# Kernel tuning notes

Hardware: AMD Instinct MI355X
Metric: run time of the kernel (lower is better)

Reference implementation:

```python
import jax, jax.numpy as jnp
import numpy as np

ALPHA = 0.929
BETA = 15.99
TAU = 0.0
EPS = 1e-8


def setup_inputs() -> dict:
    key = jax.random.key(0)
    k1, k2 = jax.random.split(key)
    head_outputs = jax.random.normal(k1, (8, 2048, 16, 128), dtype=jnp.float32)
    G = jax.random.normal(k2, (16, 16), dtype=jnp.float32)
    return {"head_outputs": head_outputs, "G": G}


def reference(head_outputs, G):
    B, T, H, d_h = head_outputs.shape
    N = B * T
    outputs = head_outputs.reshape(N, H, d_h)
    mu = outputs.mean(axis=0, keepdims=True)
    # torch .std() is unbiased (ddof=1)
    sigma = outputs.std(axis=0, keepdims=True, ddof=1)
    O_tilde = (outputs - mu) / (sigma + EPS)  # (N, H, d_h)

    # All pairwise cross-correlations in one batched contraction: (H, H, d_h, d_h)
    C = jnp.einsum('nid,nje->ijde', O_tilde, O_tilde) / N
    diff = C - jnp.eye(d_h, dtype=C.dtype)  # subtract_identity=True
    pair_loss = jnp.sum(diff * diff, axis=(2, 3))  # (H, H)

    w = ALPHA + (1.0 - ALPHA) * jax.nn.softplus(-BETA * (G - TAU))  # (H, H)

    upper = jnp.triu(jnp.ones((H, H), dtype=C.dtype), k=1)  # i < j mask
    n_pairs = H * (H - 1) // 2
    loss = jnp.sum(upper * w * pair_loss) / n_pairs
    return loss
```

## Files before the change

### kernel.cpp

```cpp
#include <hip/hip_runtime.h>
#include <hip/hip_bf16.h>

#define N_TOK   16384
#define HDIM    2048
#define NH      16
#define DH      128
#define NPAIRS  120
#define KCHUNKS 4
#define NKT     (N_TOK / 64)
#define KT_PER_CHUNK (NKT / KCHUNKS)
#define KT128_PER_CHUNK (KT_PER_CHUNK / 2)
#define PANEL_BYTES 8192

#define SUM_OFF    0u
#define SUMSQ_OFF  8192u
#define PC_OFF     36864u
#define XT_OFF     31494144u

typedef float f32x4 __attribute__((ext_vector_type(4)));
typedef int   v8i   __attribute__((ext_vector_type(8)));
typedef int   v2i   __attribute__((ext_vector_type(2)));
typedef long long i64t;

#if __has_builtin(__builtin_amdgcn_cvt_pk_fp8_f32)
__device__ __forceinline__ unsigned pk4_fp8(float a, float b, float c, float d) {
    int w = __builtin_amdgcn_cvt_pk_fp8_f32(a, b, 0, false);
    w = __builtin_amdgcn_cvt_pk_fp8_f32(c, d, w, true);
    return (unsigned)w;
}
#else
__device__ __forceinline__ unsigned char f2e4m3_sw(float f) {
    unsigned u = __float_as_uint(f);
    unsigned s = (u >> 24) & 0x80u;
    unsigned a = u & 0x7fffffffu;
    if (a >= 0x43e00000u) return (unsigned char)(s | 0x7eu);
    if (a < 0x3c800000u) {
        float av = __uint_as_float(a);
        int q = (int)rintf(av * 512.0f);
        return (unsigned char)(s | (unsigned)q);
    }
    unsigned lsb = (a >> 20) & 1u;
    a += 0x7ffffu + lsb;
    int e8 = (int)(a >> 23) - 120;
    unsigned m = (a >> 20) & 7u;
    return (unsigned char)(s | ((unsigned)e8 << 3) | m);
}
__device__ __forceinline__ unsigned pk4_fp8(float a, float b, float c, float d) {
    return (unsigned)f2e4m3_sw(a) | ((unsigned)f2e4m3_sw(b) << 8) |
           ((unsigned)f2e4m3_sw(c) << 16) | ((unsigned)f2e4m3_sw(d) << 24);
}
#endif

__global__ __launch_bounds__(256)
void stats_transpose_kernel(const float* __restrict__ X,
                            float* __restrict__ sum, float* __restrict__ sumsq,
                            unsigned char* __restrict__ Xt) {
    __shared__ float tile[64][129];
    __shared__ float sred[4][32][8];
    const int h  = blockIdx.x;
    const int by = blockIdx.y;
    const int n0 = by * 64;
    const int tx = threadIdx.x;
    const int w  = tx >> 6, l = tx & 63;
    const int cq = tx & 31;
    const int rq0 = tx >> 5;

    float4 s  = make_float4(0.f, 0.f, 0.f, 0.f);
    float4 ss = make_float4(0.f, 0.f, 0.f, 0.f);
    #pragma unroll
    for (int it = 0; it < 8; ++it) {
        int r = it * 8 + rq0;
        float4 x = *(const float4*)(X + (size_t)(n0 + r) * HDIM + h * DH + cq * 4);
        s.x += x.x; s.y += x.y; s.z += x.z; s.w += x.w;
        ss.x += x.x * x.x; ss.y += x.y * x.y; ss.z += x.z * x.z; ss.w += x.w * x.w;
        tile[r][cq * 4 + 0] = x.x; tile[r][cq * 4 + 1] = x.y;
        tile[r][cq * 4 + 2] = x.z; tile[r][cq * 4 + 3] = x.w;
    }
    s.x += __shfl_down(s.x, 32);  s.y += __shfl_down(s.y, 32);
    s.z += __shfl_down(s.z, 32);  s.w += __shfl_down(s.w, 32);
    ss.x += __shfl_down(ss.x, 32); ss.y += __shfl_down(ss.y, 32);
    ss.z += __shfl_down(ss.z, 32); ss.w += __shfl_down(ss.w, 32);
    if (l < 32) {
        sred[w][l][0] = s.x;  sred[w][l][1] = s.y;
        sred[w][l][2] = s.z;  sred[w][l][3] = s.w;
        sred[w][l][4] = ss.x; sred[w][l][5] = ss.y;
        sred[w][l][6] = ss.z; sred[w][l][7] = ss.w;
    }
    __syncthreads();
    if (tx < 32) {
        float a0 = 0.f, a1 = 0.f, a2 = 0.f, a3 = 0.f;
        float b0 = 0.f, b1 = 0.f, b2 = 0.f, b3 = 0.f;
        #pragma unroll
        for (int w2 = 0; w2 < 4; ++w2) {
            a0 += sred[w2][tx][0]; a1 += sred[w2][tx][1];
            a2 += sred[w2][tx][2]; a3 += sred[w2][tx][3];
            b0 += sred[w2][tx][4]; b1 += sred[w2][tx][5];
            b2 += sred[w2][tx][6]; b3 += sred[w2][tx][7];
        }
        int c = h * DH + tx * 4;
        atomicAdd(&sum[c + 0], a0);  atomicAdd(&sum[c + 1], a1);
        atomicAdd(&sum[c + 2], a2);  atomicAdd(&sum[c + 3], a3);
        atomicAdd(&sumsq[c + 0], b0); atomicAdd(&sumsq[c + 1], b1);
        atomicAdd(&sumsq[c + 2], b2); atomicAdd(&sumsq[c + 3], b3);
    }
    unsigned char* panel = Xt + ((size_t)h * NKT + by) * PANEL_BYTES;
    #pragma unroll
    for (int it = 0; it < 2; ++it) {
        int q = it * 256 + tx;
        int c = q >> 2, o = q & 3;
        uint4 pk;
        pk.x = pk4_fp8(tile[o*16+ 0][c], tile[o*16+ 1][c], tile[o*16+ 2][c], tile[o*16+ 3][c]);
        pk.y = pk4_fp8(tile[o*16+ 4][c], tile[o*16+ 5][c], tile[o*16+ 6][c], tile[o*16+ 7][c]);
        pk.z = pk4_fp8(tile[o*16+ 8][c], tile[o*16+ 9][c], tile[o*16+10][c], tile[o*16+11][c]);
        pk.w = pk4_fp8(tile[o*16+12][c], tile[o*16+13][c], tile[o*16+14][c], tile[o*16+15][c]);
        uint4 outv = ((c >> 3) & 1) ? make_uint4(pk.z, pk.w, pk.x, pk.y) : pk;
        *(uint4*)(panel + c * 64 + o * 16) = outv;
    }
}

__device__ __forceinline__ void gload16(const void* gsrc, void* ldst) {
    __builtin_amdgcn_global_load_lds(
        (const __attribute__((address_space(1))) unsigned int*)gsrc,
        (__attribute__((address_space(3))) unsigned int*)ldst,
        16, 0, 0);
}

__device__ __forceinline__ v8i gather_frag(const unsigned char* rp,
                                           int o0, int o1, int o2, int o3) {
    v2i x0 = *(const v2i*)(rp + o0);
    v2i x1 = *(const v2i*)(rp + o1);
    v2i x2 = *(const v2i*)(rp + o2);
    v2i x3 = *(const v2i*)(rp + o3);
    v8i r;
    r[0] = x0[0]; r[1] = x0[1];
    r[2] = x1[0]; r[3] = x1[1];
    r[4] = x2[0]; r[5] = x2[1];
    r[6] = x3[0]; r[7] = x3[1];
    return r;
}

__global__ __launch_bounds__(512, 2)
void gram_kernel(const unsigned char* __restrict__ Xt, float* __restrict__ pairP) {
    const int kc = blockIdx.x;
    const int p  = blockIdx.y;
    int i = 0, rem = p;
    while (rem >= NH - 1 - i) { rem -= NH - 1 - i; ++i; }
    const int j = i + 1 + rem;

    __shared__ alignas(16) unsigned char lds[2 * 4 * PANEL_BYTES];

    const int tx = threadIdx.x;
    const int w  = tx >> 6, l = tx & 63;
    const int wm = w >> 2, wn = w & 3;
    const int l15 = l & 15, quad = l >> 4;

    unsigned int goff;
    {
        int r0 = tx >> 2, cl0 = tx & 3;
        goff = (unsigned int)(r0 * 64 + (cl0 ^ ((r0 >> 1) & 3)) * 16);
    }
    const int lo = w * 1024;
    const char* Abase = (const char*)Xt + ((size_t)i * NKT + (size_t)kc * KT_PER_CHUNK) * PANEL_BYTES;
    const char* Bbase = (const char*)Xt + ((size_t)j * NKT + (size_t)kc * KT_PER_CHUNK) * PANEL_BYTES;

    auto STAGE = [&](int kt2, char* base) {
        const char* pa = Abase + (size_t)(kt2 * 2) * PANEL_BYTES;
        const char* pb = Bbase + (size_t)(kt2 * 2) * PANEL_BYTES;
        gload16(pa + goff,               base + lo);
        gload16(pa + PANEL_BYTES + goff, base + PANEL_BYTES + lo);
        gload16(pb + goff,               base + 2 * PANEL_BYTES + lo);
        gload16(pb + PANEL_BYTES + goff, base + 3 * PANEL_BYTES + lo);
    };

    f32x4 acc[4][2];
    #pragma unroll
    for (int mi = 0; mi < 4; ++mi)
        #pragma unroll
        for (int ni = 0; ni < 2; ++ni)
            acc[mi][ni] = (f32x4){0.f, 0.f, 0.f, 0.f};

    const int usw = (l15 & 6) | (l15 >> 3);
    const int selP = quad >> 1;
    const int ub   = (quad & 1) * 4;
    const int puo0 = ((ub + 0) ^ usw) * 8;
    const int puo1 = ((ub + 1) ^ usw) * 8;
    const int puo2 = ((ub + 2) ^ usw) * 8;
    const int puo3 = ((ub + 3) ^ usw) * 8;
    const int offA = selP * PANEL_BYTES + (wm * 64 + l15) * 64;
    const int offB = 2 * PANEL_BYTES + selP * PANEL_BYTES + (wn * 32 + l15) * 64;

    STAGE(0, (char*)lds);
    asm volatile("s_waitcnt vmcnt(0)\n\ts_barrier" ::: "memory");

    int cur = 0;
    for (int kt = 0; kt < KT128_PER_CHUNK; ++kt) {
        if (kt + 1 < KT128_PER_CHUNK)
            STAGE(kt + 1, (char*)lds + (cur ^ 1) * (4 * PANEL_BYTES));

        const unsigned char* bufb = lds + cur * (4 * PANEL_BYTES);
        const unsigned char* laP = bufb + offA;
        const unsigned char* lbP = bufb + offB;

        __builtin_amdgcn_s_setprio(1);
        v8i a0 = gather_frag(laP + 0 * 1024, puo0, puo1, puo2, puo3);
        v8i a1 = gather_frag(laP + 1 * 1024, puo0, puo1, puo2, puo3);
        v8i a2 = gather_frag(laP + 2 * 1024, puo0, puo1, puo2, puo3);
        v8i a3 = gather_frag(laP + 3 * 1024, puo0, puo1, puo2, puo3);
        #pragma unroll
        for (int ni = 0; ni < 2; ++ni) {
            v8i b = gather_frag(lbP + ni * 1024, puo0, puo1, puo2, puo3);
            acc[0][ni] = __builtin_amdgcn_mfma_scale_f32_16x16x128_f8f6f4(
                a0, b, acc[0][ni], 0, 0, 0, 0x7F7F7F7F, 0, 0x7F7F7F7F);
            acc[1][ni] = __builtin_amdgcn_mfma_scale_f32_16x16x128_f8f6f4(
                a1, b, acc[1][ni], 0, 0, 0, 0x7F7F7F7F, 0, 0x7F7F7F7F);
            acc[2][ni] = __builtin_amdgcn_mfma_scale_f32_16x16x128_f8f6f4(
                a2, b, acc[2][ni], 0, 0, 0, 0x7F7F7F7F, 0, 0x7F7F7F7F);
            acc[3][ni] = __builtin_amdgcn_mfma_scale_f32_16x16x128_f8f6f4(
                a3, b, acc[3][ni], 0, 0, 0, 0x7F7F7F7F, 0, 0x7F7F7F7F);
        }
        __builtin_amdgcn_s_setprio(0);

        if (kt + 1 < KT128_PER_CHUNK)
            asm volatile("s_waitcnt vmcnt(0) lgkmcnt(0)\n\ts_barrier" ::: "memory");
        cur ^= 1;
    }

    float* pc = pairP + ((size_t)kc * NPAIRS + (size_t)p) * (DH * DH);
    #pragma unroll
    for (int mi = 0; mi < 4; ++mi)
        #pragma unroll
        for (int ni = 0; ni < 2; ++ni)
            #pragma unroll
            for (int r = 0; r < 4; ++r) {
                int row = wm * 64 + mi * 16 + quad * 4 + r;
                int col = wn * 32 + ni * 16 + l15;
                pc[row * DH + col] = acc[mi][ni][r];
            }
}

__global__ void pair_reduce_kernel(const float* __restrict__ pairP, const float* __restrict__ G,
                                   const float* __restrict__ sum, const float* __restrict__ sumsq,
                                   float* __restrict__ out) {
    int p = blockIdx.x;
    int i = 0, rem = p;
    while (rem >= NH - 1 - i) { rem -= NH - 1 - i; ++i; }
    int j = i + 1 + rem;
    __shared__ float smui[DH], smuj[DH], sri[DH], srj[DH];
    {
        int t = threadIdx.x;
        int head = (t < DH) ? i : j;
        int d = t & (DH - 1);
        int c = head * DH + d;
        float m = sum[c] * (1.f / (float)N_TOK);
        float var = (sumsq[c] - (float)N_TOK * m * m) * (1.f / (float)(N_TOK - 1));
        var = fmaxf(var, 0.f);
        float r = 1.f / (sqrtf(var) + 1e-8f);
        if (t < DH) { smui[d] = m; sri[d] = r; }
        else        { smuj[d] = m; srj[d] = r; }
    }
    __syncthreads();
    const float invN = 1.f / (float)N_TOK;
    const size_t SLAB = (size_t)NPAIRS * DH * DH;
    const float* base = pairP + (size_t)p * (DH * DH);
    float s = 0.f;
    for (int q = threadIdx.x; q < (DH * DH) / 4; q += 256) {
        float4 v = ((const float4*)base)[q];
        #pragma unroll
        for (int kc = 1; kc < KCHUNKS; ++kc) {
            float4 t = ((const float4*)(base + kc * SLAB))[q];
            v.x += t.x; v.y += t.y; v.z += t.z; v.w += t.w;
        }
        int d = q >> 5;
        int e0 = (q & 31) * 4;
        float md = smui[d], rd = sri[d];
        float cn, df;
        cn = (v.x * invN - md * smuj[e0 + 0]) * rd * srj[e0 + 0];
        df = cn - ((d == e0 + 0) ? 1.f : 0.f); s += df * df;
        cn = (v.y * invN - md * smuj[e0 + 1]) * rd * srj[e0 + 1];
        df = cn - ((d == e0 + 1) ? 1.f : 0.f); s += df * df;
        cn = (v.z * invN - md * smuj[e0 + 2]) * rd * srj[e0 + 2];
        df = cn - ((d == e0 + 2) ? 1.f : 0.f); s += df * df;
        cn = (v.w * invN - md * smuj[e0 + 3]) * rd * srj[e0 + 3];
        df = cn - ((d == e0 + 3) ? 1.f : 0.f); s += df * df;
    }
    for (int o = 32; o; o >>= 1) s += __shfl_down(s, o);
    __shared__ float red[4];
    if ((threadIdx.x & 63) == 0) red[threadIdx.x >> 6] = s;
    __syncthreads();
    if (threadIdx.x == 0) {
        float t = red[0] + red[1] + red[2] + red[3];
        float x = -15.99f * (G[i * NH + j] - 0.0f);
        float sp = (x > 20.f) ? x : log1pf(expf(x));
        float wgt = 0.929f + (1.f - 0.929f) * sp;
        atomicAdd(out, wgt * t * (1.f / (float)NPAIRS));
    }
}

extern "C" void kernel_launch(void* const* d_in, const int* in_sizes, int n_in,
                              void* d_out, int out_size, void* d_ws, size_t ws_size,
                              hipStream_t stream) {
    const float* X = (const float*)d_in[0];
    const float* G = (const float*)d_in[1];
    float* out = (float*)d_out;
    char* ws = (char*)d_ws;

    float*         sum   = (float*)(ws + SUM_OFF);
    float*         sumsq = (float*)(ws + SUMSQ_OFF);
    float*         pairP = (float*)(ws + PC_OFF);
    unsigned char* Xt    = (unsigned char*)(ws + XT_OFF);

    hipMemsetAsync(ws + SUM_OFF, 0, 16384, stream);
    hipMemsetAsync(d_out, 0, 4, stream);

    stats_transpose_kernel<<<dim3(16, 256), 256, 0, stream>>>(X, sum, sumsq, Xt);
    gram_kernel<<<dim3(KCHUNKS, NPAIRS), 512, 0, stream>>>(Xt, pairP);
    pair_reduce_kernel<<<NPAIRS, 256, 0, stream>>>(pairP, G, sum, sumsq, out);
}
```

Baseline: 243.1 us.

## Switch Gram kernel to 32x32x64 FP8 MFMA with 4-slot LDS pipeline

Replaces the 16x16x128 scaled FP8 MFMA tiling with 32x32x64 instructions, so each wave issues two larger MFMAs per 64-wide k-step and loads fewer fragments. Staging moves from double-buffered 128-wide k-steps to a 4-slot ring of 64-wide panels with three stages in flight, waiting on vmcnt(4) instead of draining all loads. The aim is better operand reuse per LDS read and more load/compute overlap. The trade-off is a barrier on every 64-wide step, plus the ring issues wrapped-around prefetches past the end of the chunk that are loaded but never used.

```diff
diff --git a/kernel.cpp b/kernel.cpp
--- a/kernel.cpp
+++ b/kernel.cpp
@@ -9,7 +9,7 @@
 #define KCHUNKS 4
 #define NKT     (N_TOK / 64)
 #define KT_PER_CHUNK (NKT / KCHUNKS)
-#define KT128_PER_CHUNK (KT_PER_CHUNK / 2)
+#define SKT     KT_PER_CHUNK
 #define PANEL_BYTES 8192
 
 #define SUM_OFF    0u
@@ -17,9 +17,10 @@
 #define PC_OFF     36864u
 #define XT_OFF     31494144u
 
-typedef float f32x4 __attribute__((ext_vector_type(4)));
-typedef int   v8i   __attribute__((ext_vector_type(8)));
-typedef int   v2i   __attribute__((ext_vector_type(2)));
+typedef float f32x4  __attribute__((ext_vector_type(4)));
+typedef float f32x16 __attribute__((ext_vector_type(16)));
+typedef int   v8i    __attribute__((ext_vector_type(8)));
+typedef int   v2i    __attribute__((ext_vector_type(2)));
 typedef long long i64t;
 
 #if __has_builtin(__builtin_amdgcn_cvt_pk_fp8_f32)
@@ -147,12 +148,12 @@
     while (rem >= NH - 1 - i) { rem -= NH - 1 - i; ++i; }
     const int j = i + 1 + rem;
 
-    __shared__ alignas(16) unsigned char lds[2 * 4 * PANEL_BYTES];
+    __shared__ alignas(16) unsigned char lds[4 * 2 * PANEL_BYTES];
 
     const int tx = threadIdx.x;
     const int w  = tx >> 6, l = tx & 63;
     const int wm = w >> 2, wn = w & 3;
-    const int l15 = l & 15, quad = l >> 4;
+    const int l31 = l & 31, half = l >> 5;
 
     unsigned int goff;
     {
@@ -163,79 +164,57 @@
     const char* Abase = (const char*)Xt + ((size_t)i * NKT + (size_t)kc * KT_PER_CHUNK) * PANEL_BYTES;
     const char* Bbase = (const char*)Xt + ((size_t)j * NKT + (size_t)kc * KT_PER_CHUNK) * PANEL_BYTES;
 
-    auto STAGE = [&](int kt2, char* base) {
-        const char* pa = Abase + (size_t)(kt2 * 2) * PANEL_BYTES;
-        const char* pb = Bbase + (size_t)(kt2 * 2) * PANEL_BYTES;
-        gload16(pa + goff,               base + lo);
-        gload16(pa + PANEL_BYTES + goff, base + PANEL_BYTES + lo);
-        gload16(pb + goff,               base + 2 * PANEL_BYTES + lo);
-        gload16(pb + PANEL_BYTES + goff, base + 3 * PANEL_BYTES + lo);
+    auto STAGE = [&](int s, int slot) {
+        const char* pa = Abase + (size_t)s * PANEL_BYTES;
+        const char* pb = Bbase + (size_t)s * PANEL_BYTES;
+        char* base = (char*)lds + slot * (2 * PANEL_BYTES);
+        gload16(pa + goff, base + lo);
+        gload16(pb + goff, base + PANEL_BYTES + lo);
     };
 
-    f32x4 acc[4][2];
-    #pragma unroll
-    for (int mi = 0; mi < 4; ++mi)
-        #pragma unroll
-        for (int ni = 0; ni < 2; ++ni)
-            acc[mi][ni] = (f32x4){0.f, 0.f, 0.f, 0.f};
-
-    const int usw = (l15 & 6) | (l15 >> 3);
-    const int selP = quad >> 1;
-    const int ub   = (quad & 1) * 4;
-    const int puo0 = ((ub + 0) ^ usw) * 8;
-    const int puo1 = ((ub + 1) ^ usw) * 8;
-    const int puo2 = ((ub + 2) ^ usw) * 8;
-    const int puo3 = ((ub + 3) ^ usw) * 8;
-    const int offA = selP * PANEL_BYTES + (wm * 64 + l15) * 64;
-    const int offB = 2 * PANEL_BYTES + selP * PANEL_BYTES + (wn * 32 + l15) * 64;
-
-    STAGE(0, (char*)lds);
-    asm volatile("s_waitcnt vmcnt(0)\n\ts_barrier" ::: "memory");
-
-    int cur = 0;
-    for (int kt = 0; kt < KT128_PER_CHUNK; ++kt) {
-        if (kt + 1 < KT128_PER_CHUNK)
-            STAGE(kt + 1, (char*)lds + (cur ^ 1) * (4 * PANEL_BYTES));
-
-        const unsigned char* bufb = lds + cur * (4 * PANEL_BYTES);
-        const unsigned char* laP = bufb + offA;
-        const unsigned char* lbP = bufb + offB;
-
+    f32x16 acc0, acc1;
+    #pragma unroll
+    for (int e = 0; e < 16; ++e) { acc0[e] = 0.f; acc1[e] = 0.f; }
+
+    const int usw = (l31 & 6) | ((l31 >> 3) & 1);
+    const int puo0 = (((half * 4) + 0) ^ usw) * 8;
+    const int puo1 = (((half * 4) + 1) ^ usw) * 8;
+    const int puo2 = (((half * 4) + 2) ^ usw) * 8;
+    const int puo3 = (((half * 4) + 3) ^ usw) * 8;
+    const int offA0 = (wm * 64 +  0 + l31) * 64;
+    const int offA1 = (wm * 64 + 32 + l31) * 64;
+    const int offB  = PANEL_BYTES + (wn * 32 + l31) * 64;
+
+    STAGE(0, 0); STAGE(1, 1); STAGE(2, 2);
+    asm volatile("s_waitcnt vmcnt(4)\n\ts_barrier" ::: "memory");
+
+    for (int s = 0; s < SKT; ++s) {
+        STAGE((s + 3) & (SKT - 1), (s + 3) & 3);
+
+        const unsigned char* sb = lds + (s & 3) * (2 * PANEL_BYTES);
         __builtin_amdgcn_s_setprio(1);
-        v8i a0 = gather_frag(laP + 0 * 1024, puo0, puo1, puo2, puo3);
-        v8i a1 = gather_frag(laP + 1 * 1024, puo0, puo1, puo2, puo3);
-        v8i a2 = gather_frag(laP + 2 * 1024, puo0, puo1, puo2, puo3);
-        v8i a3 = gather_frag(laP + 3 * 1024, puo0, puo1, puo2, puo3);
-        #pragma unroll
-        for (int ni = 0; ni < 2; ++ni) {
-            v8i b = gather_frag(lbP + ni * 1024, puo0, puo1, puo2, puo3);
-            acc[0][ni] = __builtin_amdgcn_mfma_scale_f32_16x16x128_f8f6f4(
-                a0, b, acc[0][ni], 0, 0, 0, 0x7F7F7F7F, 0, 0x7F7F7F7F);
-            acc[1][ni] = __builtin_amdgcn_mfma_scale_f32_16x16x128_f8f6f4(
-                a1, b, acc[1][ni], 0, 0, 0, 0x7F7F7F7F, 0, 0x7F7F7F7F);
-            acc[2][ni] = __builtin_amdgcn_mfma_scale_f32_16x16x128_f8f6f4(
-                a2, b, acc[2][ni], 0, 0, 0, 0x7F7F7F7F, 0, 0x7F7F7F7F);
-            acc[3][ni] = __builtin_amdgcn_mfma_scale_f32_16x16x128_f8f6f4(
-                a3, b, acc[3][ni], 0, 0, 0, 0x7F7F7F7F, 0, 0x7F7F7F7F);
-        }
+        v8i a0 = gather_frag(sb + offA0, puo0, puo1, puo2, puo3);
+        v8i a1 = gather_frag(sb + offA1, puo0, puo1, puo2, puo3);
+        v8i b  = gather_frag(sb + offB,  puo0, puo1, puo2, puo3);
+        acc0 = __builtin_amdgcn_mfma_scale_f32_32x32x64_f8f6f4(
+            a0, b, acc0, 0, 0, 0, 0x7F7F7F7F, 0, 0x7F7F7F7F);
+        acc1 = __builtin_amdgcn_mfma_scale_f32_32x32x64_f8f6f4(
+            a1, b, acc1, 0, 0, 0, 0x7F7F7F7F, 0, 0x7F7F7F7F);
         __builtin_amdgcn_s_setprio(0);
 
-        if (kt + 1 < KT128_PER_CHUNK)
-            asm volatile("s_waitcnt vmcnt(0) lgkmcnt(0)\n\ts_barrier" ::: "memory");
-        cur ^= 1;
-    }
+        asm volatile("s_waitcnt vmcnt(4) lgkmcnt(0)\n\ts_barrier" ::: "memory");
+    }
+    asm volatile("s_waitcnt vmcnt(0)" ::: "memory");
 
     float* pc = pairP + ((size_t)kc * NPAIRS + (size_t)p) * (DH * DH);
     #pragma unroll
-    for (int mi = 0; mi < 4; ++mi)
-        #pragma unroll
-        for (int ni = 0; ni < 2; ++ni)
-            #pragma unroll
-            for (int r = 0; r < 4; ++r) {
-                int row = wm * 64 + mi * 16 + quad * 4 + r;
-                int col = wn * 32 + ni * 16 + l15;
-                pc[row * DH + col] = acc[mi][ni][r];
-            }
+    for (int e = 0; e < 16; ++e) {
+        int rl = (e & 3) + 8 * (e >> 2) + 4 * half;
+        int row = wm * 64 + rl;
+        int col = wn * 32 + l31;
+        pc[row * DH + col]        = acc0[e];
+        pc[(row + 32) * DH + col] = acc1[e];
+    }
 }
 
 __global__ void pair_reduce_kernel(const float* __restrict__ pairP, const float* __restrict__ G,
```

New measurement: 239.9 us. No clear change (-1.3%).
